# Optimization experiments

Hardware: AMD Instinct MI355X
Metric: run time of the kernel (lower is better)

Reference implementation:

```python
import jax, jax.numpy as jnp
import numpy as np

T, C, H, W, D = 100, 2, 128, 128, 8192


def setup_inputs() -> dict:
    key = jax.random.key(0)
    k1, k2, k3, k4 = jax.random.split(key, 4)
    # event histogram: nonnegative intensities per (time, polarity, y, x)
    hist = jax.random.uniform(k1, (T, C, H, W), dtype=jnp.float32)
    # torchhd Random(vsa='MAP') tables are random bipolar {-1,+1} vectors
    time_w = jnp.sign(jax.random.normal(k2, (T, D), dtype=jnp.float32))
    pol_w = jnp.sign(jax.random.normal(k3, (C, D), dtype=jnp.float32))
    pos_w = jnp.sign(jax.random.normal(k4, (H * W, D), dtype=jnp.float32))
    return {"hist": hist, "time_w": time_w, "pol_w": pol_w, "pos_w": pos_w}


def reference(hist, time_w, pol_w, pos_w):
    # Original: for every nonzero pixel, bind (elementwise mul in MAP)
    # pos_hv * pol_hv * time_hv, scale by intensity, accumulate, then sign.
    # Equivalent fused form:
    #   out_d = sign( sum_{t,p,n} hist[t,p,n] * pos_w[n,d] * pol_w[p,d] * time_w[t,d] )
    t, c, h, w = hist.shape
    flat = hist.reshape(t, c, h * w)                      # [T, 2, H*W]
    # intensity-weighted sum of position HVs per (t, p): one GEMM over H*W
    acc = jnp.einsum('tpn,nd->tpd', flat, pos_w)          # [T, 2, D]
    # bind with polarity and time HVs, reduce over t and p
    gesture = jnp.einsum('tpd,pd,td->d', acc, pol_w, time_w)  # [D]
    return jnp.sign(gesture)
```

## Files before the change

kernel.cpp:

```cpp
#include <hip/hip_runtime.h>
#include <cstdint>
#include <cstddef>

#define MROWS 200
#define PM    224
#define KDIM  16384
#define DDIM  8192
#define KSL   8
#define KPER  (KDIM / KSL)
#define BK    32
#define NSTEP (KPER / BK)

typedef __bf16 bf16x8 __attribute__((ext_vector_type(8)));
typedef float  f32x4  __attribute__((ext_vector_type(4)));

static __device__ __forceinline__ unsigned short f2bf_rne(float f) {
    unsigned int u = __float_as_uint(f);
    unsigned int r = (u + 0x7FFFu + ((u >> 16) & 1u)) >> 16;
    return (unsigned short)r;
}
static __device__ __forceinline__ float bf2f(unsigned short s) {
    return __uint_as_float(((unsigned int)s) << 16);
}

static __device__ __forceinline__ void gld_lds16(const unsigned short* g,
                                                 unsigned short* l) {
    __builtin_amdgcn_global_load_lds(
        (const __attribute__((address_space(1))) unsigned int*)g,
        (__attribute__((address_space(3))) unsigned int*)l, 16, 0, 0);
}

__global__ __launch_bounds__(256) void prep_kernel(const float* __restrict__ hist,
                                                   unsigned short* __restrict__ ahi,
                                                   unsigned short* __restrict__ alo) {
    const int g  = blockIdx.x * 256 + threadIdx.x;
    const int m  = g >> 11;
    const int gc = g & 2047;
    const int f  = (m >> 1) & 3;
    const int sgc = (gc & ~3) | ((gc & 3) ^ f);
    alignas(16) unsigned short hi[8], lo[8];
    if (m < MROWS) {
        const float* src = hist + (size_t)m * KDIM + sgc * 8;
        float4 a = *(const float4*)(src);
        float4 b = *(const float4*)(src + 4);
        const float v[8] = {a.x, a.y, a.z, a.w, b.x, b.y, b.z, b.w};
#pragma unroll
        for (int i = 0; i < 8; ++i) {
            unsigned short h = f2bf_rne(v[i]);
            hi[i] = h;
            lo[i] = f2bf_rne(v[i] - bf2f(h));
        }
    } else {
#pragma unroll
        for (int i = 0; i < 8; ++i) { hi[i] = 0; lo[i] = 0; }
    }
    *(uint4*)(ahi + (size_t)g * 8) = *(const uint4*)hi;
    *(uint4*)(alo + (size_t)g * 8) = *(const uint4*)lo;
}

__global__ __launch_bounds__(256, 2)
void gemm_kernel(const unsigned short* __restrict__ ahi,
                 const unsigned short* __restrict__ alo,
                 const float* __restrict__ pos,
                 const float* __restrict__ time_w,
                 const float* __restrict__ pol_w,
                 float* __restrict__ partials) {
    __shared__ alignas(16) unsigned short As[2][2][PM * BK];
    __shared__ alignas(16) unsigned short Bs[2][128][40];
    __shared__ float sPart[128];

    const int t     = threadIdx.x;
    const int ks    = blockIdx.x;
    const int n0    = blockIdx.y * 128;
    const int kbase = ks * KPER;

    const int lane = t & 63;
    const int wv   = t >> 6;
    const int wm   = (wv & 1) * 112;
    const int wn   = (wv >> 1) * 64;
    const int l15  = lane & 15;
    const int q8   = (lane >> 4) * 8;
    const int qg   = (lane >> 4) ^ ((l15 >> 1) & 3);

    if (t < 128) sPart[t] = 0.f;

    const int lr = lane >> 2, lg = lane & 3;
    const unsigned short* gA[7];
    unsigned short* lA[2][7];
#pragma unroll
    for (int i = 0; i < 7; ++i) {
        const int cc = wv * 7 + i;
        const int pl = (cc >= 14) ? 1 : 0;
        const int ch = cc - pl * 14;
        gA[i] = (pl ? alo : ahi) + (size_t)(ch * 16 + lr) * KDIM + kbase + lg * 8;
        lA[0][i] = &As[0][pl][ch * 512];
        lA[1][i] = &As[1][pl][ch * 512];
    }

    const int bk2 = (t & 15) * 2;
    const int bnb = (t >> 4) * 8;
    const float* gB0 = pos + ((size_t)kbase + bk2) * DDIM + n0 + bnb;
    const float* gB1 = gB0 + DDIM;

    f32x4 acc[7][4];
#pragma unroll
    for (int s = 0; s < 7; ++s)
#pragma unroll
        for (int j = 0; j < 4; ++j) acc[s][j] = (f32x4){0.f, 0.f, 0.f, 0.f};

    float4 br[2][4];

    br[0][0] = *(const float4*)(gB0);
    br[0][1] = *(const float4*)(gB0 + 4);
    br[0][2] = *(const float4*)(gB1);
    br[0][3] = *(const float4*)(gB1 + 4);
    __builtin_amdgcn_sched_barrier(0);
#pragma unroll
    for (int i = 0; i < 7; ++i) gld_lds16(gA[i], lA[0][i]);
    __builtin_amdgcn_sched_barrier(0);
    {
        const size_t r1 = (size_t)BK * DDIM;
        br[1][0] = *(const float4*)(gB0 + r1);
        br[1][1] = *(const float4*)(gB0 + r1 + 4);
        br[1][2] = *(const float4*)(gB1 + r1);
        br[1][3] = *(const float4*)(gB1 + r1 + 4);
    }
    __builtin_amdgcn_sched_barrier(0);

    for (int kp = 0; kp < NSTEP; kp += 2) {
#pragma unroll
        for (int u = 0; u < 2; ++u) {
            const int kk = kp + u;

            {
                const float xv[8] = {br[u][0].x, br[u][0].y, br[u][0].z, br[u][0].w,
                                     br[u][1].x, br[u][1].y, br[u][1].z, br[u][1].w};
                const float yv[8] = {br[u][2].x, br[u][2].y, br[u][2].z, br[u][2].w,
                                     br[u][3].x, br[u][3].y, br[u][3].z, br[u][3].w};
#pragma unroll
                for (int j = 0; j < 8; ++j) {
                    unsigned int w = (__float_as_uint(xv[j]) >> 16) |
                                     (__float_as_uint(yv[j]) & 0xFFFF0000u);
                    *(unsigned int*)&Bs[u][bnb + j][bk2] = w;
                }
            }
            __builtin_amdgcn_sched_barrier(0);
            asm volatile("s_waitcnt vmcnt(4) lgkmcnt(0)" ::: "memory");
            __builtin_amdgcn_s_barrier();
            __builtin_amdgcn_sched_barrier(0);

            {
                const int koff = ((kk + 1) & (NSTEP - 1)) * BK;
#pragma unroll
                for (int i = 0; i < 7; ++i)
                    gld_lds16(gA[i] + koff, lA[u ^ 1][i]);
            }
            __builtin_amdgcn_sched_barrier(0);

            {
                const size_t roff = (size_t)((kk + 2) & (NSTEP - 1)) * BK * DDIM;
                br[u][0] = *(const float4*)(gB0 + roff);
                br[u][1] = *(const float4*)(gB0 + roff + 4);
                br[u][2] = *(const float4*)(gB1 + roff);
                br[u][3] = *(const float4*)(gB1 + roff + 4);
            }
            __builtin_amdgcn_sched_barrier(0);

            uint4 fb[4];
#pragma unroll
            for (int j = 0; j < 4; ++j)
                fb[j] = *(const uint4*)&Bs[u][wn + j * 16 + l15][q8];

            __builtin_amdgcn_s_setprio(1);
#pragma unroll
            for (int s = 0; s < 7; ++s) {
                const int mo = (wm + s * 16 + l15) * 32 + qg * 8;
                const uint4 fa0 = *(const uint4*)&As[u][0][mo];
                const uint4 fa1 = *(const uint4*)&As[u][1][mo];
#pragma unroll
                for (int j = 0; j < 4; ++j)
                    acc[s][j] = __builtin_amdgcn_mfma_f32_16x16x32_bf16(
                        __builtin_bit_cast(bf16x8, fa0),
                        __builtin_bit_cast(bf16x8, fb[j]), acc[s][j], 0, 0, 0);
#pragma unroll
                for (int j = 0; j < 4; ++j)
                    acc[s][j] = __builtin_amdgcn_mfma_f32_16x16x32_bf16(
                        __builtin_bit_cast(bf16x8, fa1),
                        __builtin_bit_cast(bf16x8, fb[j]), acc[s][j], 0, 0, 0);
            }
            __builtin_amdgcn_s_setprio(0);
            __builtin_amdgcn_sched_barrier(0);
        }
    }

    const int qrow = (lane >> 4) * 4;
#pragma unroll
    for (int j = 0; j < 4; ++j) {
        const int col = wn + j * 16 + l15;
        const int d   = n0 + col;
        const float p0 = pol_w[d];
        const float p1 = pol_w[DDIM + d];
        float part = 0.f;
#pragma unroll
        for (int s = 0; s < 7; ++s)
#pragma unroll
            for (int r = 0; r < 4; ++r) {
                const int m = wm + s * 16 + qrow + r;
                if (m < MROWS) {
                    const float w = time_w[(size_t)(m >> 1) * DDIM + d] *
                                    ((m & 1) ? p1 : p0);
                    part += w * acc[s][j][r];
                }
            }
        atomicAdd(&sPart[col], part);
    }
    __syncthreads();
    if (t < 128) partials[(size_t)ks * DDIM + n0 + t] = sPart[t];
}

__global__ __launch_bounds__(256) void sign_reduce_kernel(const float* __restrict__ partials,
                                                          float* __restrict__ out) {
    const int d = blockIdx.x * 256 + threadIdx.x;
    float s = 0.f;
#pragma unroll
    for (int k = 0; k < KSL; ++k) s += partials[(size_t)k * DDIM + d];
    out[d] = (s > 0.f) ? 1.f : ((s < 0.f) ? -1.f : 0.f);
}

extern "C" void kernel_launch(void* const* d_in, const int* in_sizes, int n_in,
                              void* d_out, int out_size, void* d_ws, size_t ws_size,
                              hipStream_t stream) {
    const float* hist   = (const float*)d_in[0];
    const float* time_w = (const float*)d_in[1];
    const float* pol_w  = (const float*)d_in[2];
    const float* pos_w  = (const float*)d_in[3];
    float* out = (float*)d_out;

    unsigned short* ahi = (unsigned short*)d_ws;
    unsigned short* alo = ahi + (size_t)PM * KDIM;
    float* partials = (float*)(alo + (size_t)PM * KDIM);
    (void)in_sizes; (void)n_in; (void)out_size; (void)ws_size;

    prep_kernel<<<(PM * (KDIM / 8)) / 256, 256, 0, stream>>>(hist, ahi, alo);
    gemm_kernel<<<dim3(KSL, DDIM / 128), 256, 0, stream>>>(ahi, alo, pos_w,
                                                           time_w, pol_w, partials);
    sign_reduce_kernel<<<DDIM / 256, 256, 0, stream>>>(partials, out);
}
```

Baseline: 724.1 us.

## Split hi/lo bf16 planes across separate blocks and single-buffer B prefetch

Each GEMM block now processes only the hi or the lo bf16 plane of the histogram, doubling the grid and writing twice as many partial sums, which the sign-reduce kernel then adds up. This halves the A shared-memory footprint and the register state per block, raising launch bounds to three blocks per CU for more occupancy. The B register prefetch drops from two stages to one, and the custom waitcnt is replaced by a plain __syncthreads. In exchange each pos_w tile is loaded and converted twice (once per plane), and the prefetch distance is shorter.

```diff
diff --git a/kernel.cpp b/kernel.cpp
--- a/kernel.cpp
+++ b/kernel.cpp
@@ -58,21 +58,24 @@
     *(uint4*)(alo + (size_t)g * 8) = *(const uint4*)lo;
 }
 
-__global__ __launch_bounds__(256, 2)
+__global__ __launch_bounds__(256, 3)
 void gemm_kernel(const unsigned short* __restrict__ ahi,
                  const unsigned short* __restrict__ alo,
                  const float* __restrict__ pos,
                  const float* __restrict__ time_w,
                  const float* __restrict__ pol_w,
                  float* __restrict__ partials) {
-    __shared__ alignas(16) unsigned short As[2][2][PM * BK];
+    __shared__ alignas(16) unsigned short As[2][PM * BK];
     __shared__ alignas(16) unsigned short Bs[2][128][40];
     __shared__ float sPart[128];
 
     const int t     = threadIdx.x;
     const int ks    = blockIdx.x;
-    const int n0    = blockIdx.y * 128;
+    const int nb    = blockIdx.y >> 1;
+    const int pl    = blockIdx.y & 1;
+    const int n0    = nb * 128;
     const int kbase = ks * KPER;
+    const unsigned short* __restrict__ ap = pl ? alo : ahi;
 
     const int lane = t & 63;
     const int wv   = t >> 6;
@@ -84,17 +87,16 @@
 
     if (t < 128) sPart[t] = 0.f;
 
+    const int cc0 = (wv < 2) ? wv * 4 : 8 + (wv - 2) * 3;
+    const int cnt = (wv < 2) ? 4 : 3;
     const int lr = lane >> 2, lg = lane & 3;
-    const unsigned short* gA[7];
-    unsigned short* lA[2][7];
-#pragma unroll
-    for (int i = 0; i < 7; ++i) {
-        const int cc = wv * 7 + i;
-        const int pl = (cc >= 14) ? 1 : 0;
-        const int ch = cc - pl * 14;
-        gA[i] = (pl ? alo : ahi) + (size_t)(ch * 16 + lr) * KDIM + kbase + lg * 8;
-        lA[0][i] = &As[0][pl][ch * 512];
-        lA[1][i] = &As[1][pl][ch * 512];
+    const unsigned short* gA[4];
+    int lAo[4];
+#pragma unroll
+    for (int i = 0; i < 4; ++i) {
+        const int ch = cc0 + ((i < cnt) ? i : 0);
+        gA[i]  = ap + (size_t)(ch * 16 + lr) * KDIM + kbase + lg * 8;
+        lAo[i] = ch * 512;
     }
 
     const int bk2 = (t & 15) * 2;
@@ -108,89 +110,72 @@
 #pragma unroll
         for (int j = 0; j < 4; ++j) acc[s][j] = (f32x4){0.f, 0.f, 0.f, 0.f};
 
-    float4 br[2][4];
-
-    br[0][0] = *(const float4*)(gB0);
-    br[0][1] = *(const float4*)(gB0 + 4);
-    br[0][2] = *(const float4*)(gB1);
-    br[0][3] = *(const float4*)(gB1 + 4);
+    float4 br[4];
+
+    br[0] = *(const float4*)(gB0);
+    br[1] = *(const float4*)(gB0 + 4);
+    br[2] = *(const float4*)(gB1);
+    br[3] = *(const float4*)(gB1 + 4);
     __builtin_amdgcn_sched_barrier(0);
 #pragma unroll
-    for (int i = 0; i < 7; ++i) gld_lds16(gA[i], lA[0][i]);
+    for (int i = 0; i < 4; ++i)
+        if (i < cnt) gld_lds16(gA[i], &As[0][lAo[i]]);
     __builtin_amdgcn_sched_barrier(0);
-    {
-        const size_t r1 = (size_t)BK * DDIM;
-        br[1][0] = *(const float4*)(gB0 + r1);
-        br[1][1] = *(const float4*)(gB0 + r1 + 4);
-        br[1][2] = *(const float4*)(gB1 + r1);
-        br[1][3] = *(const float4*)(gB1 + r1 + 4);
-    }
-    __builtin_amdgcn_sched_barrier(0);
-
-    for (int kp = 0; kp < NSTEP; kp += 2) {
-#pragma unroll
-        for (int u = 0; u < 2; ++u) {
-            const int kk = kp + u;
-
-            {
-                const float xv[8] = {br[u][0].x, br[u][0].y, br[u][0].z, br[u][0].w,
-                                     br[u][1].x, br[u][1].y, br[u][1].z, br[u][1].w};
-                const float yv[8] = {br[u][2].x, br[u][2].y, br[u][2].z, br[u][2].w,
-                                     br[u][3].x, br[u][3].y, br[u][3].z, br[u][3].w};
-#pragma unroll
-                for (int j = 0; j < 8; ++j) {
-                    unsigned int w = (__float_as_uint(xv[j]) >> 16) |
-                                     (__float_as_uint(yv[j]) & 0xFFFF0000u);
-                    *(unsigned int*)&Bs[u][bnb + j][bk2] = w;
-                }
+
+#pragma unroll 2
+    for (int kk = 0; kk < NSTEP; ++kk) {
+        const int u = kk & 1;
+
+        {
+            const float xv[8] = {br[0].x, br[0].y, br[0].z, br[0].w,
+                                 br[1].x, br[1].y, br[1].z, br[1].w};
+            const float yv[8] = {br[2].x, br[2].y, br[2].z, br[2].w,
+                                 br[3].x, br[3].y, br[3].z, br[3].w};
+#pragma unroll
+            for (int j = 0; j < 8; ++j) {
+                unsigned int w = (__float_as_uint(xv[j]) >> 16) |
+                                 (__float_as_uint(yv[j]) & 0xFFFF0000u);
+                *(unsigned int*)&Bs[u][bnb + j][bk2] = w;
             }
-            __builtin_amdgcn_sched_barrier(0);
-            asm volatile("s_waitcnt vmcnt(4) lgkmcnt(0)" ::: "memory");
-            __builtin_amdgcn_s_barrier();
-            __builtin_amdgcn_sched_barrier(0);
-
-            {
-                const int koff = ((kk + 1) & (NSTEP - 1)) * BK;
-#pragma unroll
-                for (int i = 0; i < 7; ++i)
-                    gld_lds16(gA[i] + koff, lA[u ^ 1][i]);
-            }
-            __builtin_amdgcn_sched_barrier(0);
-
-            {
-                const size_t roff = (size_t)((kk + 2) & (NSTEP - 1)) * BK * DDIM;
-                br[u][0] = *(const float4*)(gB0 + roff);
-                br[u][1] = *(const float4*)(gB0 + roff + 4);
-                br[u][2] = *(const float4*)(gB1 + roff);
-                br[u][3] = *(const float4*)(gB1 + roff + 4);
-            }
-            __builtin_amdgcn_sched_barrier(0);
-
-            uint4 fb[4];
+        }
+        __builtin_amdgcn_sched_barrier(0);
+        __syncthreads();
+        __builtin_amdgcn_sched_barrier(0);
+
+        {
+            const int koff = ((kk + 1) & (NSTEP - 1)) * BK;
+#pragma unroll
+            for (int i = 0; i < 4; ++i)
+                if (i < cnt) gld_lds16(gA[i] + koff, &As[u ^ 1][lAo[i]]);
+        }
+        __builtin_amdgcn_sched_barrier(0);
+
+        {
+            const size_t roff = (size_t)((kk + 1) & (NSTEP - 1)) * BK * DDIM;
+            br[0] = *(const float4*)(gB0 + roff);
+            br[1] = *(const float4*)(gB0 + roff + 4);
+            br[2] = *(const float4*)(gB1 + roff);
+            br[3] = *(const float4*)(gB1 + roff + 4);
+        }
+        __builtin_amdgcn_sched_barrier(0);
+
+        uint4 fb[4];
+#pragma unroll
+        for (int j = 0; j < 4; ++j)
+            fb[j] = *(const uint4*)&Bs[u][wn + j * 16 + l15][q8];
+
+        __builtin_amdgcn_s_setprio(1);
+#pragma unroll
+        for (int s = 0; s < 7; ++s) {
+            const uint4 fa = *(const uint4*)&As[u][(wm + s * 16 + l15) * BK + qg * 8];
 #pragma unroll
             for (int j = 0; j < 4; ++j)
-                fb[j] = *(const uint4*)&Bs[u][wn + j * 16 + l15][q8];
-
-            __builtin_amdgcn_s_setprio(1);
-#pragma unroll
-            for (int s = 0; s < 7; ++s) {
-                const int mo = (wm + s * 16 + l15) * 32 + qg * 8;
-                const uint4 fa0 = *(const uint4*)&As[u][0][mo];
-                const uint4 fa1 = *(const uint4*)&As[u][1][mo];
-#pragma unroll
-                for (int j = 0; j < 4; ++j)
-                    acc[s][j] = __builtin_amdgcn_mfma_f32_16x16x32_bf16(
-                        __builtin_bit_cast(bf16x8, fa0),
-                        __builtin_bit_cast(bf16x8, fb[j]), acc[s][j], 0, 0, 0);
-#pragma unroll
-                for (int j = 0; j < 4; ++j)
-                    acc[s][j] = __builtin_amdgcn_mfma_f32_16x16x32_bf16(
-                        __builtin_bit_cast(bf16x8, fa1),
-                        __builtin_bit_cast(bf16x8, fb[j]), acc[s][j], 0, 0, 0);
-            }
-            __builtin_amdgcn_s_setprio(0);
-            __builtin_amdgcn_sched_barrier(0);
-        }
+                acc[s][j] = __builtin_amdgcn_mfma_f32_16x16x32_bf16(
+                    __builtin_bit_cast(bf16x8, fa),
+                    __builtin_bit_cast(bf16x8, fb[j]), acc[s][j], 0, 0, 0);
+        }
+        __builtin_amdgcn_s_setprio(0);
+        __builtin_amdgcn_sched_barrier(0);
     }
 
     const int qrow = (lane >> 4) * 4;
@@ -215,7 +200,8 @@
         atomicAdd(&sPart[col], part);
     }
     __syncthreads();
-    if (t < 128) partials[(size_t)ks * DDIM + n0 + t] = sPart[t];
+    if (t < 128)
+        partials[((size_t)ks * 2 + pl) * DDIM + n0 + t] = sPart[t];
 }
 
 __global__ __launch_bounds__(256) void sign_reduce_kernel(const float* __restrict__ partials,
@@ -223,7 +209,7 @@
     const int d = blockIdx.x * 256 + threadIdx.x;
     float s = 0.f;
 #pragma unroll
-    for (int k = 0; k < KSL; ++k) s += partials[(size_t)k * DDIM + d];
+    for (int k = 0; k < KSL * 2; ++k) s += partials[(size_t)k * DDIM + d];
     out[d] = (s > 0.f) ? 1.f : ((s < 0.f) ? -1.f : 0.f);
 }
 
@@ -242,7 +228,7 @@
     (void)in_sizes; (void)n_in; (void)out_size; (void)ws_size;
 
     prep_kernel<<<(PM * (KDIM / 8)) / 256, 256, 0, stream>>>(hist, ahi, alo);
-    gemm_kernel<<<dim3(KSL, DDIM / 128), 256, 0, stream>>>(ahi, alo, pos_w,
-                                                           time_w, pol_w, partials);
+    gemm_kernel<<<dim3(KSL, 2 * (DDIM / 128)), 256, 0, stream>>>(
+        ahi, alo, pos_w, time_w, pol_w, partials);
     sign_reduce_kernel<<<DDIM / 256, 256, 0, stream>>>(partials, out);
 }
```

Result: slower. 945.1 us (+30.5%).
